# Kernel optimization log

Measured on AMD Instinct MI355X. Metric: run time of the kernel, lower is better.

The kernel has to match this reference:

```python
import jax, jax.numpy as jnp
import numpy as np

N, E, IN_FEATS, HID, HEADS = 50000, 800000, 256, 32, 8
NEG_SLOPE = 0.2


def _init_params(key):
    ks = jax.random.split(key, 12)
    def lin(k, fi, fo):
        return jax.random.normal(k, (fi, fo), jnp.float32) * (1.0 / np.sqrt(fi))
    p = {}
    # layer 0: in_feats -> HID x HEADS
    p['W0'] = lin(ks[0], IN_FEATS, HEADS * HID)
    p['al0'] = jax.random.normal(ks[1], (HEADS, HID), jnp.float32) * 0.1
    p['ar0'] = jax.random.normal(ks[2], (HEADS, HID), jnp.float32) * 0.1
    p['b0'] = jnp.zeros((HEADS * HID,), jnp.float32)
    # layer 1: HID*HEADS -> HID x HEADS
    p['W1'] = lin(ks[3], HEADS * HID, HEADS * HID)
    p['al1'] = jax.random.normal(ks[4], (HEADS, HID), jnp.float32) * 0.1
    p['ar1'] = jax.random.normal(ks[5], (HEADS, HID), jnp.float32) * 0.1
    p['b1'] = jnp.zeros((HEADS * HID,), jnp.float32)
    # layer 2 (final): HID*HEADS -> HID x 1 head, no activation
    p['W2'] = lin(ks[6], HEADS * HID, HID)
    p['al2'] = jax.random.normal(ks[7], (1, HID), jnp.float32) * 0.1
    p['ar2'] = jax.random.normal(ks[8], (1, HID), jnp.float32) * 0.1
    p['b2'] = jnp.zeros((HID,), jnp.float32)
    return p


def setup_inputs() -> dict:
    key = jax.random.key(0)
    k1, k2, k3, kp = jax.random.split(key, 4)
    inp = {
        'features': jax.random.normal(k1, (N, IN_FEATS), jnp.float32),
        'src': jax.random.randint(k2, (E,), 0, N, jnp.int32),
        'dst': jax.random.randint(k3, (E,), 0, N, jnp.int32),
    }
    inp.update(_init_params(kp))
    return inp


def _gat_layer(x, src, dst, W, al, ar, b, heads, act):
    n = x.shape[0]
    d = W.shape[1] // heads
    feat = (x @ W).reshape(n, heads, d)           # [N,H,D]
    el = jnp.sum(feat * al, axis=-1)              # [N,H]
    er = jnp.sum(feat * ar, axis=-1)              # [N,H]
    e = jax.nn.leaky_relu(el[src] + er[dst], NEG_SLOPE)   # [E,H]
    # segment softmax over destination neighborhoods
    emax = jax.ops.segment_max(e, dst, num_segments=n)
    ex = jnp.exp(e - emax[dst])
    denom = jax.ops.segment_sum(ex, dst, num_segments=n)
    a = ex / (denom[dst] + 1e-9)                  # [E,H]
    msg = feat[src] * a[:, :, None]               # [E,H,D]
    out = jax.ops.segment_sum(msg, dst, num_segments=n)   # [N,H,D]
    out = out + b.reshape(1, heads, d)
    return act(out) if act is not None else out


def reference(features, src, dst, W0, al0, ar0, b0, W1, al1, ar1, b1, W2, al2, ar2, b2):
    h = _gat_layer(features, src, dst, W0, al0, ar0, b0, HEADS, jax.nn.elu)
    h = h.reshape(h.shape[0], -1)
    h = _gat_layer(h, src, dst, W1, al1, ar1, b1, HEADS, jax.nn.elu)
    h = h.reshape(h.shape[0], -1)
    h = _gat_layer(h, src, dst, W2, al2, ar2, b2, 1, None)   # [N,1,D]
    return h.mean(axis=1)                                    # [N,D]
```

## Files before the change

### kernel.cpp

```cpp
#include <hip/hip_runtime.h>

typedef unsigned short u16;
typedef unsigned int   u32;
typedef __attribute__((ext_vector_type(8))) short  short8;
typedef __attribute__((ext_vector_type(4))) float  f32x4;
typedef __attribute__((ext_vector_type(2))) float  f32x2;
typedef __attribute__((ext_vector_type(2))) unsigned int u32v2;
typedef __attribute__((ext_vector_type(4))) unsigned int u32v4;

#define NN 50000
#define NE 800000

__device__ __forceinline__ float bf2f(u16 b) { return __uint_as_float(((u32)b) << 16); }
__device__ __forceinline__ float bflo(u32 p) { return __uint_as_float(p << 16); }
__device__ __forceinline__ float bfhi(u32 p) { return __uint_as_float(p & 0xffff0000u); }
__device__ __forceinline__ u16 f2bf(float f) {
    u32 u = __float_as_uint(f);
    u32 r = u + 0x7fffu + ((u >> 16) & 1u);
    return (u16)(r >> 16);
}
__device__ __forceinline__ float lexp(float v) {
    v = v > 0.f ? v : 0.2f * v;
    return __expf(fminf(v, 60.f));
}

struct DetectArgs { const u32* p[13]; int nw[13]; };

__global__ __launch_bounds__(256) void k_detect(DetectArgs a, int* flags) {
    __shared__ int sh[256], sz[256];
    int j = blockIdx.x;
    const u32* x = a.p[j];
    int n = a.nw[j];
    int t = threadIdx.x;
    int hits = 0, nz = 0;
    for (int i = t; i < n; i += 256) {
        u32 w = x[i];
        if (w) {
            ++nz;
            u32 e = (w >> 7) & 0xffu;
            if (e >= 100 && e <= 150) ++hits;
        }
    }
    sh[t] = hits; sz[t] = nz;
    __syncthreads();
    for (int ofs = 128; ofs > 0; ofs >>= 1) {
        if (t < ofs) { sh[t] += sh[t + ofs]; sz[t] += sz[t + ofs]; }
        __syncthreads();
    }
    if (t == 0) flags[j] = (sz[0] == 0) ? 2 : ((sh[0] * 2 >= sz[0]) ? 0 : 1);
}

struct ConvArgs { const void* s[9]; float* d[9]; int n[9]; int fi[9]; };

__global__ void k_convert(ConvArgs a, const int* __restrict__ flags) {
    int j = blockIdx.y;
    int i = blockIdx.x * 256 + threadIdx.x;
    if (i >= a.n[j]) return;
    int fl = flags[a.fi[j]];
    float v = 0.f;
    if (fl == 1) v = ((const float*)a.s[j])[i];
    else if (fl == 0) v = bf2f(((const u16*)a.s[j])[i]);
    a.d[j][i] = v;
}

__global__ void k_wpack(const void* __restrict__ Wsrc, const int* __restrict__ flags,
                        int fidx, int N, u16* __restrict__ Wp, int nchunks) {
    int id = blockIdx.x * 256 + threadIdx.x;
    if (id >= nchunks) return;
    int L = id & 63, kt = (id >> 6) & 7, nt = id >> 9;
    int col = nt * 16 + (L & 15);
    int krow = kt * 32 + ((L >> 4) & 3) * 8;
    bool isf32 = (flags[fidx] == 1);
#pragma unroll
    for (int j = 0; j < 8; ++j) {
        int s = (krow + j) * N + col;
        Wp[id * 8 + j] = isf32 ? f2bf(((const float*)Wsrc)[s]) : ((const u16*)Wsrc)[s];
    }
}

__global__ void k_hist(const int* __restrict__ dst, int* __restrict__ deg, int E) {
    int e = blockIdx.x * 256 + threadIdx.x;
    if (e < E) atomicAdd(&deg[dst[e]], 1);
}

__global__ __launch_bounds__(256) void k_scan_partial(const int* __restrict__ deg,
                                                      int* __restrict__ bsum, int n) {
    __shared__ int red[256];
    int t = threadIdx.x;
    int i = blockIdx.x * 256 + t;
    red[t] = (i < n) ? deg[i] : 0;
    __syncthreads();
    for (int ofs = 128; ofs > 0; ofs >>= 1) {
        if (t < ofs) red[t] += red[t + ofs];
        __syncthreads();
    }
    if (t == 0) bsum[blockIdx.x] = red[0];
}

__global__ __launch_bounds__(256) void k_scan_bsum(int* __restrict__ bsum, int nb) {
    __shared__ int s[256];
    int t = threadIdx.x;
    int v = (t < nb) ? bsum[t] : 0;
    s[t] = v;
    __syncthreads();
    for (int ofs = 1; ofs < 256; ofs <<= 1) {
        int x = (t >= ofs) ? s[t - ofs] : 0;
        __syncthreads();
        s[t] += x;
        __syncthreads();
    }
    if (t < nb) bsum[t] = s[t] - v;
}

__global__ __launch_bounds__(256) void k_scan_final(const int* __restrict__ deg,
                                                    const int* __restrict__ bsum,
                                                    int* __restrict__ rowptr,
                                                    int* __restrict__ cursor, int n) {
    __shared__ int s[256];
    int t = threadIdx.x;
    int i = blockIdx.x * 256 + t;
    int v = (i < n) ? deg[i] : 0;
    s[t] = v;
    __syncthreads();
    for (int ofs = 1; ofs < 256; ofs <<= 1) {
        int x = (t >= ofs) ? s[t - ofs] : 0;
        __syncthreads();
        s[t] += x;
        __syncthreads();
    }
    int excl = bsum[blockIdx.x] + s[t] - v;
    if (i < n) {
        rowptr[i] = excl;
        cursor[i] = excl;
        if (i == n - 1) rowptr[n] = excl + v;
    }
}

__global__ void k_scatter(const int* __restrict__ src, const int* __restrict__ dst,
                          int* __restrict__ cursor, int* __restrict__ csr_src, int E) {
    int e = blockIdx.x * 256 + threadIdx.x;
    if (e >= E) return;
    int p = atomicAdd(&cursor[dst[e]], 1);
    csr_src[p] = src[e];
}

__global__ __launch_bounds__(256) void k_gemm_mfma(const void* __restrict__ Xv,
                                                   const int* __restrict__ xflag,
                                                   const u16* __restrict__ Wp,
                                                   u16* __restrict__ OUT, int nrows) {
    __shared__ u16 As[64 * 256];
    const int t = threadIdx.x;
    const int w = t >> 6, L = t & 63;
    const int quad = (L >> 4) & 3;
    const int r0 = blockIdx.x * 64;
    const int nb = blockIdx.y * 8;
    const bool xf32 = (xflag != nullptr) && (*xflag == 1);

    short8* Asv = (short8*)As;
    short8 zero = {0, 0, 0, 0, 0, 0, 0, 0};
#pragma unroll
    for (int i = 0; i < 8; ++i) {
        int g = i * 256 + t;
        int row = g >> 5, cc = g & 31;
        int r = r0 + row;
        short8 val = zero;
        if (r < nrows) {
            if (xf32) {
                const f32x4* Xf4 = (const f32x4*)Xv;
                f32x4 lo = Xf4[(size_t)r * 64 + cc * 2];
                f32x4 hi = Xf4[(size_t)r * 64 + cc * 2 + 1];
                val[0] = (short)f2bf(lo[0]); val[1] = (short)f2bf(lo[1]);
                val[2] = (short)f2bf(lo[2]); val[3] = (short)f2bf(lo[3]);
                val[4] = (short)f2bf(hi[0]); val[5] = (short)f2bf(hi[1]);
                val[6] = (short)f2bf(hi[2]); val[7] = (short)f2bf(hi[3]);
            } else {
                val = ((const short8*)Xv)[(size_t)r * 32 + cc];
            }
        }
        Asv[cc * 64 + row] = val;
    }

    const short8* Wv = (const short8*)Wp;
    short8 bf[2][8];
#pragma unroll
    for (int jn = 0; jn < 2; ++jn) {
        int nt = nb + w + jn * 4;
#pragma unroll
        for (int kt = 0; kt < 8; ++kt) bf[jn][kt] = Wv[(nt * 8 + kt) * 64 + L];
    }
    __syncthreads();

    f32x4 acc[4][2];
#pragma unroll
    for (int mi = 0; mi < 4; ++mi)
#pragma unroll
        for (int jn = 0; jn < 2; ++jn) acc[mi][jn] = (f32x4){0.f, 0.f, 0.f, 0.f};

#pragma unroll
    for (int kt = 0; kt < 8; ++kt) {
#pragma unroll
        for (int mi = 0; mi < 4; ++mi) {
            short8 af = Asv[(kt * 4 + quad) * 64 + mi * 16 + (L & 15)];
            acc[mi][0] = __builtin_amdgcn_mfma_f32_16x16x32_bf16(af, bf[0][kt], acc[mi][0], 0, 0, 0);
            acc[mi][1] = __builtin_amdgcn_mfma_f32_16x16x32_bf16(af, bf[1][kt], acc[mi][1], 0, 0, 0);
        }
    }

    const int colbase = blockIdx.y * 128;
#pragma unroll
    for (int mi = 0; mi < 4; ++mi) {
        int rb = r0 + mi * 16 + quad * 4;
#pragma unroll
        for (int jn = 0; jn < 2; ++jn) {
            int c = colbase + (w + jn * 4) * 16 + (L & 15);
#pragma unroll
            for (int reg = 0; reg < 4; ++reg) {
                int r = rb + reg;
                if (r < nrows) OUT[(size_t)r * 256 + c] = f2bf(acc[mi][jn][reg]);
            }
        }
    }
}

__global__ __launch_bounds__(256) void k_gemm_mfma32(const u16* __restrict__ Xb,
                                                     const u16* __restrict__ Wp,
                                                     u16* __restrict__ OUT, int nrows) {
    __shared__ u16 As[128 * 256];
    const int t = threadIdx.x;
    const int w = t >> 6, L = t & 63;
    const int quad = (L >> 4) & 3;
    const int r0 = blockIdx.x * 128;
    const int mh = (w >> 1) * 64, nt = w & 1;

    const short8* Xv = (const short8*)Xb;
    short8* Asv = (short8*)As;
    short8 zero = {0, 0, 0, 0, 0, 0, 0, 0};
#pragma unroll
    for (int i = 0; i < 16; ++i) {
        int g = i * 256 + t;
        int row = g >> 5, cc = g & 31;
        int r = r0 + row;
        Asv[cc * 128 + row] = (r < nrows) ? Xv[(size_t)r * 32 + cc] : zero;
    }

    const short8* Wv = (const short8*)Wp;
    short8 bf[8];
#pragma unroll
    for (int kt = 0; kt < 8; ++kt) bf[kt] = Wv[(nt * 8 + kt) * 64 + L];
    __syncthreads();

    f32x4 acc[4];
#pragma unroll
    for (int mi = 0; mi < 4; ++mi) acc[mi] = (f32x4){0.f, 0.f, 0.f, 0.f};

#pragma unroll
    for (int kt = 0; kt < 8; ++kt) {
#pragma unroll
        for (int mi = 0; mi < 4; ++mi) {
            short8 af = Asv[(kt * 4 + quad) * 128 + mh + mi * 16 + (L & 15)];
            acc[mi] = __builtin_amdgcn_mfma_f32_16x16x32_bf16(af, bf[kt], acc[mi], 0, 0, 0);
        }
    }

#pragma unroll
    for (int mi = 0; mi < 4; ++mi) {
        int rb = r0 + mh + mi * 16 + quad * 4;
        int c = nt * 16 + (L & 15);
#pragma unroll
        for (int reg = 0; reg < 4; ++reg) {
            int r = rb + reg;
            if (r < nrows) OUT[(size_t)r * 32 + c] = f2bf(acc[mi][reg]);
        }
    }
}

__global__ void k_elr8(const u16* __restrict__ featb, const float* __restrict__ al,
                       const float* __restrict__ ar, float* __restrict__ el,
                       float* __restrict__ er, int n) {
    int idx = blockIdx.x * 256 + threadIdx.x;
    if (idx >= n * 8) return;
    int node = idx >> 3, h = idx & 7;
    const u32v4* fu = (const u32v4*)((const u32*)featb + (size_t)node * 128 + h * 16);
    const float* A = al + h * 32;
    const float* B = ar + h * 32;
    float sl = 0.f, sr = 0.f;
#pragma unroll
    for (int j = 0; j < 4; ++j) {
        u32v4 w4 = fu[j];
#pragma unroll
        for (int k = 0; k < 4; ++k) {
            u32 w = (k == 0) ? w4.x : (k == 1) ? w4.y : (k == 2) ? w4.z : w4.w;
            float f0 = bflo(w), f1 = bfhi(w);
            int c = j * 8 + k * 2;
            sl += f0 * A[c] + f1 * A[c + 1];
            sr += f0 * B[c] + f1 * B[c + 1];
        }
    }
    el[idx] = sl;
    er[idx] = sr;
}

__global__ void k_elr1(const u16* __restrict__ featb, const float* __restrict__ al,
                       const float* __restrict__ ar, float* __restrict__ el,
                       float* __restrict__ er, int n) {
    int node = blockIdx.x * 256 + threadIdx.x;
    if (node >= n) return;
    const u32v4* fu = (const u32v4*)((const u32*)featb + (size_t)node * 16);
    float sl = 0.f, sr = 0.f;
#pragma unroll
    for (int j = 0; j < 4; ++j) {
        u32v4 w4 = fu[j];
#pragma unroll
        for (int k = 0; k < 4; ++k) {
            u32 w = (k == 0) ? w4.x : (k == 1) ? w4.y : (k == 2) ? w4.z : w4.w;
            float f0 = bflo(w), f1 = bfhi(w);
            int c = j * 8 + k * 2;
            sl += f0 * al[c] + f1 * al[c + 1];
            sr += f0 * ar[c] + f1 * ar[c + 1];
        }
    }
    el[node] = sl;
    er[node] = sr;
}

__global__ __launch_bounds__(256) void k_gather8(const int* __restrict__ rowptr,
                                                 const int* __restrict__ csr_src,
                                                 const float* __restrict__ el,
                                                 const float* __restrict__ er,
                                                 const u32v2* __restrict__ featb4,
                                                 const float* __restrict__ bias,
                                                 u32v2* __restrict__ xout4) {
    int t = threadIdx.x;
    int d = blockIdx.x * 4 + (t >> 6);
    int q = t & 63;
    int h = q >> 3;
    int b = rowptr[d], e = rowptr[d + 1];
    float erd = er[d * 8 + h];
    float a0 = 0.f, a1 = 0.f, a2 = 0.f, a3 = 0.f, ssum = 0.f;
    int p = b;
    for (; p + 4 <= e; p += 4) {
        int s0 = csr_src[p], s1 = csr_src[p + 1], s2 = csr_src[p + 2], s3 = csr_src[p + 3];
        float e0 = lexp(el[s0 * 8 + h] + erd);
        float e1 = lexp(el[s1 * 8 + h] + erd);
        float e2 = lexp(el[s2 * 8 + h] + erd);
        float e3 = lexp(el[s3 * 8 + h] + erd);
        u32v2 w0 = featb4[(size_t)s0 * 64 + q];
        u32v2 w1 = featb4[(size_t)s1 * 64 + q];
        u32v2 w2 = featb4[(size_t)s2 * 64 + q];
        u32v2 w3 = featb4[(size_t)s3 * 64 + q];
        a0 += bflo(w0.x) * e0; a1 += bfhi(w0.x) * e0; a2 += bflo(w0.y) * e0; a3 += bfhi(w0.y) * e0;
        a0 += bflo(w1.x) * e1; a1 += bfhi(w1.x) * e1; a2 += bflo(w1.y) * e1; a3 += bfhi(w1.y) * e1;
        a0 += bflo(w2.x) * e2; a1 += bfhi(w2.x) * e2; a2 += bflo(w2.y) * e2; a3 += bfhi(w2.y) * e2;
        a0 += bflo(w3.x) * e3; a1 += bfhi(w3.x) * e3; a2 += bflo(w3.y) * e3; a3 += bfhi(w3.y) * e3;
        ssum += (e0 + e1) + (e2 + e3);
    }
    for (; p < e; ++p) {
        int s = csr_src[p];
        float ev = lexp(el[s * 8 + h] + erd);
        u32v2 w = featb4[(size_t)s * 64 + q];
        a0 += bflo(w.x) * ev; a1 += bfhi(w.x) * ev;
        a2 += bflo(w.y) * ev; a3 += bfhi(w.y) * ev;
        ssum += ev;
    }
    float rd = 1.f / (ssum + 1e-9f);
    const float4 bb = *(const float4*)&bias[4 * q];
    float v0 = a0 * rd + bb.x;
    float v1 = a1 * rd + bb.y;
    float v2 = a2 * rd + bb.z;
    float v3 = a3 * rd + bb.w;
    v0 = v0 > 0.f ? v0 : expm1f(v0);
    v1 = v1 > 0.f ? v1 : expm1f(v1);
    v2 = v2 > 0.f ? v2 : expm1f(v2);
    v3 = v3 > 0.f ? v3 : expm1f(v3);
    u32v2 o;
    o.x = (u32)f2bf(v0) | ((u32)f2bf(v1) << 16);
    o.y = (u32)f2bf(v2) | ((u32)f2bf(v3) << 16);
    xout4[(size_t)d * 64 + q] = o;
}

__global__ __launch_bounds__(256) void k_gather1(const int* __restrict__ rowptr,
                                                 const int* __restrict__ csr_src,
                                                 const float* __restrict__ el,
                                                 const float* __restrict__ er,
                                                 const u32* __restrict__ featb2,
                                                 const float* __restrict__ bias,
                                                 void* __restrict__ out,
                                                 const int* __restrict__ flag, int n) {
    int t = threadIdx.x;
    int d = blockIdx.x * 16 + (t >> 4);
    int q = t & 15;
    if (d >= n) return;
    int b = rowptr[d], e = rowptr[d + 1];
    float erd = er[d];
    float a0 = 0.f, a1 = 0.f, ssum = 0.f;
    int p = b;
    for (; p + 4 <= e; p += 4) {
        int s0 = csr_src[p], s1 = csr_src[p + 1], s2 = csr_src[p + 2], s3 = csr_src[p + 3];
        float e0 = lexp(el[s0] + erd);
        float e1 = lexp(el[s1] + erd);
        float e2 = lexp(el[s2] + erd);
        float e3 = lexp(el[s3] + erd);
        u32 w0 = featb2[(size_t)s0 * 16 + q];
        u32 w1 = featb2[(size_t)s1 * 16 + q];
        u32 w2 = featb2[(size_t)s2 * 16 + q];
        u32 w3 = featb2[(size_t)s3 * 16 + q];
        a0 += bflo(w0) * e0; a1 += bfhi(w0) * e0;
        a0 += bflo(w1) * e1; a1 += bfhi(w1) * e1;
        a0 += bflo(w2) * e2; a1 += bfhi(w2) * e2;
        a0 += bflo(w3) * e3; a1 += bfhi(w3) * e3;
        ssum += (e0 + e1) + (e2 + e3);
    }
    for (; p < e; ++p) {
        int s = csr_src[p];
        float ev = lexp(el[s] + erd);
        u32 w = featb2[(size_t)s * 16 + q];
        a0 += bflo(w) * ev;
        a1 += bfhi(w) * ev;
        ssum += ev;
    }
    float rd = 1.f / (ssum + 1e-9f);
    float v0 = a0 * rd + bias[2 * q];
    float v1 = a1 * rd + bias[2 * q + 1];
    if (*flag == 1) {
        f32x2 o = {v0, v1};
        ((f32x2*)out)[(size_t)d * 16 + q] = o;
    } else {
        ((u32*)out)[(size_t)d * 16 + q] = (u32)f2bf(v0) | ((u32)f2bf(v1) << 16);
    }
}

extern "C" void kernel_launch(void* const* d_in, const int* in_sizes, int n_in,
                              void* d_out, int out_size, void* d_ws, size_t ws_size,
                              hipStream_t stream) {
    const void* features = d_in[0];
    const int* src = (const int*)d_in[1];
    const int* dst = (const int*)d_in[2];

    char* ws = (char*)d_ws;
    size_t off = 0;
    auto carve = [&](size_t bytes) -> void* {
        void* p = ws + off;
        off = (off + bytes + 255) & ~(size_t)255;
        return p;
    };
    int*   flags = (int*)carve(64);
    float* pconv = (float*)carve(2048 * 4);
    u16*   Wp0 = (u16*)carve(65536 * 2);
    u16*   Wp1 = (u16*)carve(65536 * 2);
    u16*   Wp2 = (u16*)carve(8192 * 2);
    u16*   Xb    = (u16*)carve((size_t)NN * 256 * 2);
    u16*   featb = (u16*)carve((size_t)NN * 256 * 2);
    float* el   = (float*)carve((size_t)NN * 8 * 4);
    float* er   = (float*)carve((size_t)NN * 8 * 4);
    int*   deg     = (int*)carve((size_t)NN * 4);
    int*   cursor  = (int*)carve((size_t)NN * 4);
    int*   rowptr  = (int*)carve((size_t)(NN + 1) * 4);
    int*   bsum    = (int*)carve(256 * 4);
    int*   csr_src = (int*)carve((size_t)NE * 4);
    if (off > ws_size) return;

    const int N = NN, E = NE;
    const int nscan = (N + 255) / 256;

    DetectArgs da;
    const int din_idx[13] = {0, 3, 4, 5, 6, 7, 8, 9, 10, 11, 12, 13, 14};
    for (int j = 0; j < 13; ++j) {
        da.p[j] = (const u32*)d_in[din_idx[j]];
        int nw = in_sizes[din_idx[j]] / 2;
        da.nw[j] = nw > 512 ? 512 : nw;
    }
    k_detect<<<13, 256, 0, stream>>>(da, flags);

    ConvArgs ca;
    const int psl[9] = {4, 5, 6, 8, 9, 10, 12, 13, 14};
    const int pfl[9] = {2, 3, 4, 6, 7, 8, 10, 11, 12};
    float* dsts[9];
    {
        size_t o = 0;
        for (int j = 0; j < 9; ++j) {
            dsts[j] = pconv + o;
            o += (size_t)in_sizes[psl[j]];
        }
    }
    for (int j = 0; j < 9; ++j) {
        ca.s[j] = d_in[psl[j]];
        ca.d[j] = dsts[j];
        ca.n[j] = in_sizes[psl[j]];
        ca.fi[j] = pfl[j];
    }
    k_convert<<<dim3(1, 9), 256, 0, stream>>>(ca, flags);
    float* al0f = dsts[0]; float* ar0f = dsts[1]; float* b0f = dsts[2];
    float* al1f = dsts[3]; float* ar1f = dsts[4]; float* b1f = dsts[5];
    float* al2f = dsts[6]; float* ar2f = dsts[7]; float* b2f = dsts[8];

    k_wpack<<<32, 256, 0, stream>>>(d_in[3],  flags, 1, 256, Wp0, 8192);
    k_wpack<<<32, 256, 0, stream>>>(d_in[7],  flags, 5, 256, Wp1, 8192);
    k_wpack<<<4,  256, 0, stream>>>(d_in[11], flags, 9, 32,  Wp2, 1024);

    hipMemsetAsync(deg, 0, (size_t)N * 4, stream);
    k_hist<<<(E + 255) / 256, 256, 0, stream>>>(dst, deg, E);
    k_scan_partial<<<nscan, 256, 0, stream>>>(deg, bsum, N);
    k_scan_bsum<<<1, 256, 0, stream>>>(bsum, nscan);
    k_scan_final<<<nscan, 256, 0, stream>>>(deg, bsum, rowptr, cursor, N);
    k_scatter<<<(E + 255) / 256, 256, 0, stream>>>(src, dst, cursor, csr_src, E);

    const dim3 ggrid((N + 63) / 64, 2);

    k_gemm_mfma<<<ggrid, 256, 0, stream>>>(features, flags, Wp0, featb, N);
    k_elr8<<<(N * 8 + 255) / 256, 256, 0, stream>>>(featb, al0f, ar0f, el, er, N);
    k_gather8<<<N / 4, 256, 0, stream>>>(rowptr, csr_src, el, er,
                                         (const u32v2*)featb, b0f, (u32v2*)Xb);

    k_gemm_mfma<<<ggrid, 256, 0, stream>>>(Xb, nullptr, Wp1, featb, N);
    k_elr8<<<(N * 8 + 255) / 256, 256, 0, stream>>>(featb, al1f, ar1f, el, er, N);
    k_gather8<<<N / 4, 256, 0, stream>>>(rowptr, csr_src, el, er,
                                         (const u32v2*)featb, b1f, (u32v2*)Xb);

    k_gemm_mfma32<<<(N + 127) / 128, 256, 0, stream>>>(Xb, Wp2, featb, N);
    k_elr1<<<(N + 255) / 256, 256, 0, stream>>>(featb, al2f, ar2f, el, er, N);
    k_gather1<<<(N + 15) / 16, 256, 0, stream>>>(rowptr, csr_src, el, er,
                                                 (const u32*)featb, b2f,
                                                 d_out, flags, N);
}
```

Measured before the change: 444.7 us.

## Software-pipeline 8-head gather with cooperative attention compute in 8-edge chunks

Rewrites the 8-head aggregation kernel to process neighbors in chunks of 8 edges. Each lane computes the attention exponential once for a distinct (edge, head) pair, and the results are shared through LDS instead of every feature lane recomputing them. Source indices and feature rows for the next chunk are prefetched while the current chunk accumulates. The softmax denominator is reduced with wave shuffles. In exchange it adds more registers, LDS traffic and intra-wave LDS communication without an explicit barrier, and the padded edges in partial chunks issue redundant feature loads.

```diff
diff --git a/kernel.cpp b/kernel.cpp
--- a/kernel.cpp
+++ b/kernel.cpp
@@ -20,7 +20,7 @@
     return (u16)(r >> 16);
 }
 __device__ __forceinline__ float lexp(float v) {
-    v = v > 0.f ? v : 0.2f * v;
+    v = fmaxf(v, 0.2f * v);
     return __expf(fminf(v, 60.f));
 }
 
@@ -330,39 +330,110 @@
                                                  const u32v2* __restrict__ featb4,
                                                  const float* __restrict__ bias,
                                                  u32v2* __restrict__ xout4) {
-    int t = threadIdx.x;
-    int d = blockIdx.x * 4 + (t >> 6);
-    int q = t & 63;
-    int h = q >> 3;
-    int b = rowptr[d], e = rowptr[d + 1];
-    float erd = er[d * 8 + h];
-    float a0 = 0.f, a1 = 0.f, a2 = 0.f, a3 = 0.f, ssum = 0.f;
-    int p = b;
-    for (; p + 4 <= e; p += 4) {
-        int s0 = csr_src[p], s1 = csr_src[p + 1], s2 = csr_src[p + 2], s3 = csr_src[p + 3];
-        float e0 = lexp(el[s0 * 8 + h] + erd);
-        float e1 = lexp(el[s1 * 8 + h] + erd);
-        float e2 = lexp(el[s2 * 8 + h] + erd);
-        float e3 = lexp(el[s3 * 8 + h] + erd);
-        u32v2 w0 = featb4[(size_t)s0 * 64 + q];
-        u32v2 w1 = featb4[(size_t)s1 * 64 + q];
-        u32v2 w2 = featb4[(size_t)s2 * 64 + q];
-        u32v2 w3 = featb4[(size_t)s3 * 64 + q];
-        a0 += bflo(w0.x) * e0; a1 += bfhi(w0.x) * e0; a2 += bflo(w0.y) * e0; a3 += bfhi(w0.y) * e0;
-        a0 += bflo(w1.x) * e1; a1 += bfhi(w1.x) * e1; a2 += bflo(w1.y) * e1; a3 += bfhi(w1.y) * e1;
-        a0 += bflo(w2.x) * e2; a1 += bfhi(w2.x) * e2; a2 += bflo(w2.y) * e2; a3 += bfhi(w2.y) * e2;
-        a0 += bflo(w3.x) * e3; a1 += bfhi(w3.x) * e3; a2 += bflo(w3.y) * e3; a3 += bfhi(w3.y) * e3;
-        ssum += (e0 + e1) + (e2 + e3);
-    }
-    for (; p < e; ++p) {
-        int s = csr_src[p];
-        float ev = lexp(el[s * 8 + h] + erd);
-        u32v2 w = featb4[(size_t)s * 64 + q];
-        a0 += bflo(w.x) * ev; a1 += bfhi(w.x) * ev;
-        a2 += bflo(w.y) * ev; a3 += bfhi(w.y) * ev;
-        ssum += ev;
-    }
-    float rd = 1.f / (ssum + 1e-9f);
+    __shared__ __align__(16) float sAL[4][2][64];
+    __shared__ __align__(16) int   sSL[4][2][8];
+    const int t = threadIdx.x;
+    const int wv = t >> 6;
+    const int q = t & 63;
+    const int d = blockIdx.x * 4 + wv;
+    const int eL = q >> 3, hL = q & 7;
+    const int b = rowptr[d], e = rowptr[d + 1];
+    const int deg = e - b;
+    const int nch = (deg + 7) >> 3;
+    const float erA = er[d * 8 + hL];
+
+    float (*AL)[64] = sAL[wv];
+    int (*SL)[8] = sSL[wv];
+
+    float a0 = 0.f, a1 = 0.f, a2 = 0.f, a3 = 0.f;
+    float partial = 0.f;
+
+    u32v2 fw[8], fw2[8];
+    int csrP = 0, ncP = 0;
+    float elP = 0.f;
+
+    if (nch > 0) {
+        const int nc0 = deg < 8 ? deg : 8;
+        const int i0 = eL < nc0 ? eL : nc0 - 1;
+        const int s0 = csr_src[b + i0];
+        if (nch > 1) {
+            const int r1 = deg - 8;
+            ncP = r1 < 8 ? r1 : 8;
+            const int i1 = eL < ncP ? eL : ncP - 1;
+            csrP = csr_src[b + 8 + i1];
+        }
+        const float el0 = el[s0 * 8 + hL];
+        if (hL == 0) SL[0][eL] = s0;
+        const int4 sv0 = *(const int4*)&SL[0][0];
+        const int4 sv1 = *(const int4*)&SL[0][4];
+        fw[0] = featb4[sv0.x * 64 + q];
+        fw[1] = featb4[sv0.y * 64 + q];
+        fw[2] = featb4[sv0.z * 64 + q];
+        fw[3] = featb4[sv0.w * 64 + q];
+        fw[4] = featb4[sv1.x * 64 + q];
+        fw[5] = featb4[sv1.y * 64 + q];
+        fw[6] = featb4[sv1.z * 64 + q];
+        fw[7] = featb4[sv1.w * 64 + q];
+        const float ex0 = (eL < nc0) ? lexp(el0 + erA) : 0.f;
+        partial += ex0;
+        AL[0][hL * 8 + eL] = ex0;
+        if (nch > 1) elP = el[csrP * 8 + hL];
+    }
+
+    for (int c = 0; c < nch; ++c) {
+        const int cur = c & 1, nxt = cur ^ 1;
+
+        int csrF = 0, ncF = 0;
+        if (c + 2 < nch) {
+            const int r2 = deg - (c + 2) * 8;
+            ncF = r2 < 8 ? r2 : 8;
+            const int i2 = eL < ncF ? eL : ncF - 1;
+            csrF = csr_src[b + (c + 2) * 8 + i2];
+        }
+
+        if (c + 1 < nch) {
+            if (hL == 0) SL[nxt][eL] = csrP;
+            const int4 sv0 = *(const int4*)&SL[nxt][0];
+            const int4 sv1 = *(const int4*)&SL[nxt][4];
+            fw2[0] = featb4[sv0.x * 64 + q];
+            fw2[1] = featb4[sv0.y * 64 + q];
+            fw2[2] = featb4[sv0.z * 64 + q];
+            fw2[3] = featb4[sv0.w * 64 + q];
+            fw2[4] = featb4[sv1.x * 64 + q];
+            fw2[5] = featb4[sv1.y * 64 + q];
+            fw2[6] = featb4[sv1.z * 64 + q];
+            fw2[7] = featb4[sv1.w * 64 + q];
+            const float exN = (eL < ncP) ? lexp(elP + erA) : 0.f;
+            partial += exN;
+            AL[nxt][hL * 8 + eL] = exN;
+        }
+
+        const int h8 = (q >> 3) * 8;
+        const f32x4 A0 = *(const f32x4*)&AL[cur][h8];
+        const f32x4 A1 = *(const f32x4*)&AL[cur][h8 + 4];
+
+        if (c + 2 < nch) elP = el[csrF * 8 + hL];
+
+#define GAT_EDGE(i, axv) { const u32v2 w_ = fw[i]; \
+        a0 += bflo(w_.x) * (axv); a1 += bfhi(w_.x) * (axv); \
+        a2 += bflo(w_.y) * (axv); a3 += bfhi(w_.y) * (axv); }
+        GAT_EDGE(0, A0[0]) GAT_EDGE(1, A0[1]) GAT_EDGE(2, A0[2]) GAT_EDGE(3, A0[3])
+        GAT_EDGE(4, A1[0]) GAT_EDGE(5, A1[1]) GAT_EDGE(6, A1[2]) GAT_EDGE(7, A1[3])
+#undef GAT_EDGE
+
+#pragma unroll
+        for (int i = 0; i < 8; ++i) fw[i] = fw2[i];
+        csrP = csrF;
+        ncP = ncF;
+    }
+
+    float v = partial;
+    v += __shfl_xor(v, 8);
+    v += __shfl_xor(v, 16);
+    v += __shfl_xor(v, 32);
+    const float ssd = __shfl(v, q >> 3);
+
+    const float rd = 1.f / (ssd + 1e-9f);
     const float4 bb = *(const float4*)&bias[4 * q];
     float v0 = a0 * rd + bb.x;
     float v1 = a1 * rd + bb.y;
@@ -375,7 +446,7 @@
     u32v2 o;
     o.x = (u32)f2bf(v0) | ((u32)f2bf(v1) << 16);
     o.y = (u32)f2bf(v2) | ((u32)f2bf(v3) << 16);
-    xout4[(size_t)d * 64 + q] = o;
+    xout4[d * 64 + q] = o;
 }
 
 __global__ __launch_bounds__(256) void k_gather1(const int* __restrict__ rowptr,
```

After: 442.7 us. About the same (-0.4%).
